# Kernel optimization log

Hardware: AMD Instinct MI355X
Metric: run time of the kernel (lower is better)

Reference implementation:

```python
import jax, jax.numpy as jnp
import numpy as np

BATCH = 2048
K = 64          # num_clusters
D = 128         # latent_dim / cluster_dim
R1 = 1024
OUT_LEN = 512   # output_length
IN_LEN = 512    # input_length
MIN_CLAMP = 0.0


def setup_inputs() -> dict:
    key = jax.random.key(0)
    k1, k2, k3, k4, k5, k6 = jax.random.split(key, 6)
    z = jax.random.normal(k1, (BATCH, 1, D), dtype=jnp.float32)
    u = jax.random.normal(k2, (BATCH, 1, R1), dtype=jnp.float32)
    member = jax.random.uniform(k3, (BATCH, 1, K), dtype=jnp.float32)
    # parameters
    mu = jax.random.uniform(k4, (K, D), dtype=jnp.float32)  # 1 * torch.rand
    sigma_inv = 10.0 * jnp.broadcast_to(jnp.eye(D, dtype=jnp.float32), (K, D, D))  # zeros with diag 10
    # nn.Linear default init: U(-1/sqrt(fan_in), 1/sqrt(fan_in)), weight shape (out, in)
    bound = 1.0 / np.sqrt(R1)
    W_con = jax.random.uniform(k5, (K, OUT_LEN, R1), dtype=jnp.float32, minval=-bound, maxval=bound)
    W_recon = jax.random.uniform(k6, (K, IN_LEN, R1), dtype=jnp.float32, minval=-bound, maxval=bound)
    return {"z": z, "u": u, "member": member, "mu": mu, "sigma_inv": sigma_inv,
            "W_con": W_con, "W_recon": W_recon}


def _compute_psi(z, mu, sigma_inv):
    # z: (B,1,D), mu: (K,D) -> d: (B,K,D)
    d = mu[None, :, :] - z
    # S = sigma_inv @ sigma_inv^T per cluster: (K,D,D)
    S = jnp.einsum('kde,kfe->kdf', sigma_inv, sigma_inv)
    # Mahalanobis: d^T S d per (b,k)
    d2 = jnp.einsum('bkd,kde,bke->bk', d, S, d)
    d2 = jnp.maximum(d2, MIN_CLAMP)
    psi = jax.nn.softmax(-d2, axis=1)  # (B,K)
    return psi


def reference(z, u, member, mu, sigma_inv, W_con, W_recon):
    psi = _compute_psi(z, mu, sigma_inv)          # (B,K)
    u2 = u[:, 0, :]                                # (B,R1)
    # grouped GEMM + abs: per-cluster |Linear(u)|
    y_LLM = jnp.abs(jnp.einsum('bi,koi->bko', u2, W_con))    # (B,K,OUT_LEN)
    x_LLM = jnp.abs(jnp.einsum('bi,koi->bko', u2, W_recon))  # (B,K,IN_LEN)
    mem = member[:, 0, :]                          # (B,K)
    y_con = jnp.einsum('bk,bko->bo', psi, y_LLM)[:, None, :]   # (B,1,OUT_LEN)
    x_recon = jnp.einsum('bk,bko->bo', mem, x_LLM)[:, None, :]  # (B,1,IN_LEN)
    return (y_con, x_recon)
```

## Files before the change

### kernel.cpp

```cpp
#include <hip/hip_runtime.h>
#include <hip/hip_bf16.h>
#include <stdint.h>

typedef __bf16 bf16_t;
typedef __bf16 bf16x8 __attribute__((ext_vector_type(8)));
typedef __bf16 bf16x4 __attribute__((ext_vector_type(4)));
typedef float  v4f    __attribute__((ext_vector_type(4)));
typedef float  f32x4  __attribute__((ext_vector_type(4)));

#define GLDS16(gp, lp)                                                         \
  __builtin_amdgcn_global_load_lds(                                            \
      (__attribute__((address_space(1))) void*)(gp),                           \
      (__attribute__((address_space(3))) void*)(lp), 16, 0, 0)

#define BATCH 2048
#define KEXP  64
#define NOUT  512
#define R1    1024

__global__ __launch_bounds__(256) void cast_u_k(const float* __restrict__ u,
                                                bf16_t* __restrict__ ub) {
  int idx = blockIdx.x * 256 + threadIdx.x;
  float4 v = ((const float4*)u)[idx];
  bf16x4 o;
  o.x = (bf16_t)v.x; o.y = (bf16_t)v.y; o.z = (bf16_t)v.z; o.w = (bf16_t)v.w;
  ((bf16x4*)ub)[idx] = o;
}

__global__ __launch_bounds__(256) void cast_w_k(const float* __restrict__ wcon,
                                                const float* __restrict__ wrec,
                                                bf16_t* __restrict__ wb) {
  const size_t tid = (size_t)blockIdx.x * 256 + threadIdx.x;
#pragma unroll
  for (int it = 0; it < 8; ++it) {
    size_t idx = tid + (size_t)it * (8192u * 256u);
    size_t e = idx << 2;
    int k = (int)(e >> 20);
    int n = (int)((e >> 10) & 1023);
    int i = (int)(e & 1023);
    const float* src = (n < NOUT)
        ? (wcon + (((size_t)k * NOUT + n) << 10) + i)
        : (wrec + (((size_t)k * NOUT + (n - NOUT)) << 10) + i);
    f32x4 v = __builtin_nontemporal_load((const f32x4*)src);
    bf16x4 o;
    o.x = (bf16_t)v.x; o.y = (bf16_t)v.y; o.z = (bf16_t)v.z; o.w = (bf16_t)v.w;
    ((bf16x4*)wb)[idx] = o;
  }
}

__global__ __launch_bounds__(256) void psi_d2_k(const float* __restrict__ z,
                                                const float* __restrict__ mu,
                                                const float* __restrict__ sig,
                                                float* __restrict__ d2g) {
  __shared__ float dv[64][132];
  __shared__ float Ss[16][128];
  const int t = threadIdx.x;
  const int k = blockIdx.x;
  const int b0 = blockIdx.y * 64;

  const float* muk = mu + k * 128;
#pragma unroll
  for (int i = 0; i < 8; ++i) {
    int f4 = i * 256 + t;
    int row = f4 >> 5, c4 = f4 & 31;
    float4 zq = ((const float4*)(z + (size_t)(b0 + row) * 128))[c4];
    float4 mq = ((const float4*)muk)[c4];
    float4 dq;
    dq.x = mq.x - zq.x; dq.y = mq.y - zq.y;
    dq.z = mq.z - zq.z; dq.w = mq.w - zq.w;
    *(float4*)&dv[row][c4 * 4] = dq;
  }

  const int et = t & 15, bt = t >> 4;
  const float* Sk = sig + ((size_t)k << 14);
  float acc[4][8];
#pragma unroll
  for (int j = 0; j < 4; ++j)
#pragma unroll
    for (int i = 0; i < 8; ++i) acc[j][i] = 0.f;

  for (int dblk = 0; dblk < 8; ++dblk) {
    __syncthreads();
#pragma unroll
    for (int i = 0; i < 2; ++i) {
      int f4 = i * 256 + t;
      int row = f4 >> 5, c4 = f4 & 31;
      *(float4*)&Ss[row][c4 * 4] =
          ((const float4*)(Sk + (size_t)(dblk * 16 + row) * 128))[c4];
    }
    __syncthreads();

#pragma unroll
    for (int d4 = 0; d4 < 4; ++d4) {
      float4 a[4];
#pragma unroll
      for (int j = 0; j < 4; ++j)
        a[j] = *(const float4*)&dv[bt * 4 + j][dblk * 16 + d4 * 4];
#pragma unroll
      for (int dd = 0; dd < 4; ++dd) {
        float4 s0 = *(const float4*)&Ss[d4 * 4 + dd][et * 8];
        float4 s1 = *(const float4*)&Ss[d4 * 4 + dd][et * 8 + 4];
        float av[4] = {a[0][dd], a[1][dd], a[2][dd], a[3][dd]};
#pragma unroll
        for (int j = 0; j < 4; ++j) {
          acc[j][0] = fmaf(s0.x, av[j], acc[j][0]);
          acc[j][1] = fmaf(s0.y, av[j], acc[j][1]);
          acc[j][2] = fmaf(s0.z, av[j], acc[j][2]);
          acc[j][3] = fmaf(s0.w, av[j], acc[j][3]);
          acc[j][4] = fmaf(s1.x, av[j], acc[j][4]);
          acc[j][5] = fmaf(s1.y, av[j], acc[j][5]);
          acc[j][6] = fmaf(s1.z, av[j], acc[j][6]);
          acc[j][7] = fmaf(s1.w, av[j], acc[j][7]);
        }
      }
    }
  }

  float v2[4];
#pragma unroll
  for (int j = 0; j < 4; ++j) {
    float s = 0.f;
#pragma unroll
    for (int i = 0; i < 8; ++i) s = fmaf(acc[j][i], acc[j][i], s);
    v2[j] = s;
  }
#pragma unroll
  for (int j = 0; j < 4; ++j) {
    v2[j] += __shfl_xor(v2[j], 1);
    v2[j] += __shfl_xor(v2[j], 2);
    v2[j] += __shfl_xor(v2[j], 4);
    v2[j] += __shfl_xor(v2[j], 8);
  }
  if (et == 0) {
#pragma unroll
    for (int j = 0; j < 4; ++j)
      d2g[(size_t)(b0 + bt * 4 + j) * 64 + k] = v2[j];
  }
}

__global__ __launch_bounds__(256) void psi_sm_k(const float* __restrict__ d2g,
                                                float* __restrict__ psi) {
  const int b = blockIdx.x * 4 + (threadIdx.x >> 6);
  const int lane = threadIdx.x & 63;
  float x = fmaxf(d2g[(size_t)b * 64 + lane], 0.0f);
  float m = x;
  m = fminf(m, __shfl_xor(m, 1));  m = fminf(m, __shfl_xor(m, 2));
  m = fminf(m, __shfl_xor(m, 4));  m = fminf(m, __shfl_xor(m, 8));
  m = fminf(m, __shfl_xor(m, 16)); m = fminf(m, __shfl_xor(m, 32));
  float ex = __expf(m - x);
  float s = ex;
  s += __shfl_xor(s, 1);  s += __shfl_xor(s, 2);  s += __shfl_xor(s, 4);
  s += __shfl_xor(s, 8);  s += __shfl_xor(s, 16); s += __shfl_xor(s, 32);
  psi[(size_t)b * 64 + lane] = ex / s;
}

__global__ __launch_bounds__(256, 2)
void fused_gemm(const bf16_t* __restrict__ ub,
                const bf16_t* __restrict__ wb,
                const float* __restrict__ psi,
                const float* __restrict__ member,
                float* __restrict__ out) {
  __shared__ bf16_t Alds[2][128 * 64];
  __shared__ bf16_t Blds[2][128 * 64];
  __shared__ float  wlds[16][128];

  const int t = threadIdx.x, lane = t & 63, wv = t >> 6;
  const int rr  = blockIdx.x + (blockIdx.y << 4) + (blockIdx.z << 7);
  const int bm0 = ((rr >> 3) & 15) << 7;
  const int n0  = (rr & 7) << 7;
  const int e0  = (rr >> 7) << 4;
  const bool is_y = (n0 < NOUT);
  const float* wsel = is_y ? psi : member;
  const int wm = wv & 1, wn = wv >> 1;
  const int l15 = lane & 15, quad = lane >> 4;
  const int fsw = l15 & 7;

  v4f acc[4][4], oacc[4][4];
#pragma unroll
  for (int mi = 0; mi < 4; ++mi)
#pragma unroll
    for (int ni = 0; ni < 4; ++ni)
#pragma unroll
      for (int r = 0; r < 4; ++r) { acc[mi][ni][r] = 0.f; oacc[mi][ni][r] = 0.f; }

  const int rA = wv * 8 + (lane >> 3);
  const int c8 = (((lane & 7) ^ (lane >> 3)) * 8);
  const bf16_t* au  = ub + (size_t)(bm0 + rA) * R1 + c8;
  const bf16_t* bw0 = wb + (size_t)(n0 + rA) * R1 + c8;

  const int aoff = (wm * 64 + l15) * 64;
  const int boff = (wn * 64 + l15) * 64;
  const int co0 = (quad ^ fsw) * 8;
  const int co1 = ((4 + quad) ^ fsw) * 8;

  auto STAGE = [&](int s2, int p) {
    const int ex2 = e0 + (s2 >> 4);
    const int kk2 = (s2 & 15) << 6;
    const bf16_t* a = au + kk2;
    const bf16_t* b = bw0 + ((size_t)ex2 << 20) + kk2;
    bf16_t* Ad = &Alds[p][wv * 8 * 64];
    bf16_t* Bd = &Blds[p][wv * 8 * 64];
#pragma unroll
    for (int j = 0; j < 4; ++j)
      GLDS16(a + (size_t)(j * 32) * R1, Ad + j * 32 * 64);
#pragma unroll
    for (int j = 0; j < 4; ++j)
      GLDS16(b + (size_t)(j * 32) * R1, Bd + j * 32 * 64);
  };

  {
    const int r = t >> 1, h = (t & 1) * 8;
    const float* src = wsel + (size_t)(bm0 + r) * 64 + e0 + h;
    f32x4 v0 = *(const f32x4*)src;
    f32x4 v1 = *(const f32x4*)(src + 4);
#pragma unroll
    for (int j = 0; j < 4; ++j) { wlds[h + j][r] = v0[j]; wlds[h + 4 + j][r] = v1[j]; }
  }
  STAGE(0, 0);
  STAGE(1, 1);
  asm volatile("s_waitcnt vmcnt(8) lgkmcnt(0)" ::: "memory");
  asm volatile("s_barrier" ::: "memory");

  bf16x8 a0[4], b0[4], a1[4], b1[4];
#pragma unroll
  for (int i = 0; i < 4; ++i) {
    a0[i] = *(const bf16x8*)(&Alds[0][aoff] + i * 16 * 64 + co0);
    b0[i] = *(const bf16x8*)(&Blds[0][boff] + i * 16 * 64 + co0);
  }

  for (int ke = 0; ke < 16; ++ke) {
#pragma unroll 2
    for (int kt = 0; kt < 16; ++kt) {
      const int p = kt & 1;
      const int s = (ke << 4) + kt;
      const bf16_t* Ap = &Alds[p][aoff];
      const bf16_t* Bp = &Blds[p][boff];

#pragma unroll
      for (int i = 0; i < 4; ++i) {
        a1[i] = *(const bf16x8*)(Ap + i * 16 * 64 + co1);
        b1[i] = *(const bf16x8*)(Bp + i * 16 * 64 + co1);
      }
      asm volatile("s_waitcnt lgkmcnt(8)" ::: "memory");
      __builtin_amdgcn_sched_barrier(0);
      __builtin_amdgcn_s_setprio(1);
#pragma unroll
      for (int mi = 0; mi < 4; ++mi)
#pragma unroll
        for (int ni = 0; ni < 4; ++ni)
          acc[mi][ni] = __builtin_amdgcn_mfma_f32_16x16x32_bf16(
              a0[mi], b0[ni], acc[mi][ni], 0, 0, 0);
      __builtin_amdgcn_s_setprio(0);

      asm volatile("s_waitcnt lgkmcnt(0)" ::: "memory");
      asm volatile("s_barrier" ::: "memory");

      int s2 = s + 2; s2 = (s2 > 255) ? 255 : s2;
      STAGE(s2, p);

      asm volatile("s_waitcnt vmcnt(8)" ::: "memory");
      asm volatile("s_barrier" ::: "memory");

      const bf16_t* An = &Alds[p ^ 1][aoff];
      const bf16_t* Bn = &Blds[p ^ 1][boff];
#pragma unroll
      for (int i = 0; i < 4; ++i) {
        a0[i] = *(const bf16x8*)(An + i * 16 * 64 + co0);
        b0[i] = *(const bf16x8*)(Bn + i * 16 * 64 + co0);
      }
      __builtin_amdgcn_s_setprio(1);
#pragma unroll
      for (int mi = 0; mi < 4; ++mi)
#pragma unroll
        for (int ni = 0; ni < 4; ++ni)
          acc[mi][ni] = __builtin_amdgcn_mfma_f32_16x16x32_bf16(
              a1[mi], b1[ni], acc[mi][ni], 0, 0, 0);
      __builtin_amdgcn_s_setprio(0);
    }

#pragma unroll
    for (int mi = 0; mi < 4; ++mi) {
      float wr[4];
#pragma unroll
      for (int r = 0; r < 4; ++r)
        wr[r] = wlds[ke][wm * 64 + mi * 16 + quad * 4 + r];
#pragma unroll
      for (int ni = 0; ni < 4; ++ni)
#pragma unroll
        for (int r = 0; r < 4; ++r) {
          oacc[mi][ni][r] += fabsf(acc[mi][ni][r]) * wr[r];
          acc[mi][ni][r] = 0.f;
        }
    }
  }

  float* obase = is_y ? out : out + (size_t)BATCH * NOUT;
  const int oc = (is_y ? n0 : n0 - NOUT) + wn * 64 + l15;
#pragma unroll
  for (int mi = 0; mi < 4; ++mi)
#pragma unroll
    for (int ni = 0; ni < 4; ++ni)
#pragma unroll
      for (int r = 0; r < 4; ++r) {
        int brow = bm0 + wm * 64 + mi * 16 + quad * 4 + r;
        atomicAdd(&obase[(size_t)brow * NOUT + oc + ni * 16], oacc[mi][ni][r]);
      }
  asm volatile("s_waitcnt vmcnt(0) lgkmcnt(0)" ::: "memory");
}

extern "C" void kernel_launch(void* const* d_in, const int* in_sizes, int n_in,
                              void* d_out, int out_size, void* d_ws, size_t ws_size,
                              hipStream_t stream) {
  const float* z    = (const float*)d_in[0];
  const float* u    = (const float*)d_in[1];
  const float* mem  = (const float*)d_in[2];
  const float* mu   = (const float*)d_in[3];
  const float* sig  = (const float*)d_in[4];
  const float* wcon = (const float*)d_in[5];
  const float* wrec = (const float*)d_in[6];
  float* out = (float*)d_out;

  char* ws = (char*)d_ws;
  bf16_t* ub  = (bf16_t*)ws;
  bf16_t* wb  = (bf16_t*)(ws + ((size_t)4 << 20));
  float*  psw = (float*)(ws + ((size_t)132 << 20));
  float*  d2g = (float*)(ws + ((size_t)132 << 20) + ((size_t)512 << 10));

  hipMemsetAsync(d_out, 0, (size_t)out_size * sizeof(float), stream);
  cast_u_k<<<2048, 256, 0, stream>>>(u, ub);
  cast_w_k<<<8192, 256, 0, stream>>>(wcon, wrec, wb);
  psi_d2_k<<<dim3(64, 32), 256, 0, stream>>>(z, mu, sig, d2g);
  psi_sm_k<<<512, 256, 0, stream>>>(d2g, psw);
  fused_gemm<<<dim3(16, 8, 4), 256, 0, stream>>>(ub, wb, psw, mem, out);
}
```

Before: 642.9 us.

## Load A operand directly from global into registers, dropping A LDS staging

```diff
diff --git a/kernel.cpp b/kernel.cpp
--- a/kernel.cpp
+++ b/kernel.cpp
@@ -160,7 +160,6 @@
                 const float* __restrict__ psi,
                 const float* __restrict__ member,
                 float* __restrict__ out) {
-  __shared__ bf16_t Alds[2][128 * 64];
   __shared__ bf16_t Blds[2][128 * 64];
   __shared__ float  wlds[16][128];
 
@@ -185,27 +184,62 @@
 
   const int rA = wv * 8 + (lane >> 3);
   const int c8 = (((lane & 7) ^ (lane >> 3)) * 8);
-  const bf16_t* au  = ub + (size_t)(bm0 + rA) * R1 + c8;
   const bf16_t* bw0 = wb + (size_t)(n0 + rA) * R1 + c8;
 
-  const int aoff = (wm * 64 + l15) * 64;
+  const bf16_t* uA = ub + (size_t)(bm0 + wm * 64 + l15) * R1 + quad * 8;
+
   const int boff = (wn * 64 + l15) * 64;
   const int co0 = (quad ^ fsw) * 8;
   const int co1 = ((4 + quad) ^ fsw) * 8;
 
-  auto STAGE = [&](int s2, int p) {
+  auto STAGEB = [&](int s2, int p) {
     const int ex2 = e0 + (s2 >> 4);
     const int kk2 = (s2 & 15) << 6;
-    const bf16_t* a = au + kk2;
     const bf16_t* b = bw0 + ((size_t)ex2 << 20) + kk2;
-    bf16_t* Ad = &Alds[p][wv * 8 * 64];
     bf16_t* Bd = &Blds[p][wv * 8 * 64];
-#pragma unroll
-    for (int j = 0; j < 4; ++j)
-      GLDS16(a + (size_t)(j * 32) * R1, Ad + j * 32 * 64);
 #pragma unroll
     for (int j = 0; j < 4; ++j)
       GLDS16(b + (size_t)(j * 32) * R1, Bd + j * 32 * 64);
+  };
+
+  auto LOADA = [&](int s1, bf16x8* af) {
+    const bf16_t* ap = uA + ((s1 & 15) << 6);
+#pragma unroll
+    for (int mi = 0; mi < 4; ++mi) {
+      af[mi]     = *(const bf16x8*)(ap + (size_t)(mi * 16) * R1);
+      af[4 + mi] = *(const bf16x8*)(ap + (size_t)(mi * 16) * R1 + 32);
+    }
+  };
+
+  bf16x8 af0[8], af1[8];
+
+  auto STEP = [&](int s, int p, bf16x8* afc, bf16x8* afn) {
+    const bf16_t* Bp = &Blds[p][boff];
+    bf16x8 bfr[8];
+#pragma unroll
+    for (int i = 0; i < 4; ++i) {
+      bfr[i]     = *(const bf16x8*)(Bp + i * 16 * 64 + co0);
+      bfr[4 + i] = *(const bf16x8*)(Bp + i * 16 * 64 + co1);
+    }
+    int s1 = s + 1; if (s1 > 255) s1 = 255;
+    LOADA(s1, afn);
+    asm volatile("s_waitcnt vmcnt(12) lgkmcnt(0)" ::: "memory");
+    __builtin_amdgcn_sched_barrier(0);
+    asm volatile("s_barrier" ::: "memory");
+    int s2 = s + 2; if (s2 > 255) s2 = 255;
+    STAGEB(s2, p);
+    __builtin_amdgcn_s_setprio(1);
+#pragma unroll
+    for (int ks = 0; ks < 2; ++ks)
+#pragma unroll
+      for (int mi = 0; mi < 4; ++mi)
+#pragma unroll
+        for (int ni = 0; ni < 4; ++ni)
+          acc[mi][ni] = __builtin_amdgcn_mfma_f32_16x16x32_bf16(
+              afc[ks * 4 + mi], bfr[ks * 4 + ni], acc[mi][ni], 0, 0, 0);
+    __builtin_amdgcn_s_setprio(0);
+    asm volatile("s_waitcnt vmcnt(12)" ::: "memory");
+    asm volatile("s_barrier" ::: "memory");
   };
 
   {
@@ -216,68 +250,19 @@
 #pragma unroll
     for (int j = 0; j < 4; ++j) { wlds[h + j][r] = v0[j]; wlds[h + 4 + j][r] = v1[j]; }
   }
-  STAGE(0, 0);
-  STAGE(1, 1);
-  asm volatile("s_waitcnt vmcnt(8) lgkmcnt(0)" ::: "memory");
+  LOADA(0, af0);
+  STAGEB(0, 0);
+  STAGEB(1, 1);
+  asm volatile("s_waitcnt vmcnt(4) lgkmcnt(0)" ::: "memory");
   asm volatile("s_barrier" ::: "memory");
 
-  bf16x8 a0[4], b0[4], a1[4], b1[4];
-#pragma unroll
-  for (int i = 0; i < 4; ++i) {
-    a0[i] = *(const bf16x8*)(&Alds[0][aoff] + i * 16 * 64 + co0);
-    b0[i] = *(const bf16x8*)(&Blds[0][boff] + i * 16 * 64 + co0);
-  }
-
   for (int ke = 0; ke < 16; ++ke) {
+    const int sb = ke << 4;
 #pragma unroll 2
-    for (int kt = 0; kt < 16; ++kt) {
-      const int p = kt & 1;
-      const int s = (ke << 4) + kt;
-      const bf16_t* Ap = &Alds[p][aoff];
-      const bf16_t* Bp = &Blds[p][boff];
-
-#pragma unroll
-      for (int i = 0; i < 4; ++i) {
-        a1[i] = *(const bf16x8*)(Ap + i * 16 * 64 + co1);
-        b1[i] = *(const bf16x8*)(Bp + i * 16 * 64 + co1);
-      }
-      asm volatile("s_waitcnt lgkmcnt(8)" ::: "memory");
-      __builtin_amdgcn_sched_barrier(0);
-      __builtin_amdgcn_s_setprio(1);
-#pragma unroll
-      for (int mi = 0; mi < 4; ++mi)
-#pragma unroll
-        for (int ni = 0; ni < 4; ++ni)
-          acc[mi][ni] = __builtin_amdgcn_mfma_f32_16x16x32_bf16(
-              a0[mi], b0[ni], acc[mi][ni], 0, 0, 0);
-      __builtin_amdgcn_s_setprio(0);
-
-      asm volatile("s_waitcnt lgkmcnt(0)" ::: "memory");
-      asm volatile("s_barrier" ::: "memory");
-
-      int s2 = s + 2; s2 = (s2 > 255) ? 255 : s2;
-      STAGE(s2, p);
-
-      asm volatile("s_waitcnt vmcnt(8)" ::: "memory");
-      asm volatile("s_barrier" ::: "memory");
-
-      const bf16_t* An = &Alds[p ^ 1][aoff];
-      const bf16_t* Bn = &Blds[p ^ 1][boff];
-#pragma unroll
-      for (int i = 0; i < 4; ++i) {
-        a0[i] = *(const bf16x8*)(An + i * 16 * 64 + co0);
-        b0[i] = *(const bf16x8*)(Bn + i * 16 * 64 + co0);
-      }
-      __builtin_amdgcn_s_setprio(1);
-#pragma unroll
-      for (int mi = 0; mi < 4; ++mi)
-#pragma unroll
-        for (int ni = 0; ni < 4; ++ni)
-          acc[mi][ni] = __builtin_amdgcn_mfma_f32_16x16x32_bf16(
-              a1[mi], b1[ni], acc[mi][ni], 0, 0, 0);
-      __builtin_amdgcn_s_setprio(0);
-    }
-
+    for (int kt = 0; kt < 16; kt += 2) {
+      STEP(sb + kt,     0, af0, af1);
+      STEP(sb + kt + 1, 1, af1, af0);
+    }
 #pragma unroll
     for (int mi = 0; mi < 4; ++mi) {
       float wr[4];
```

Measured after the change: 919.1 us. +43.0%, slower.

## Restructure Mahalanobis kernel to read sigma via wave-uniform scalar loads

Applied to the files above, without the earlier changes.

```diff
diff --git a/kernel.cpp b/kernel.cpp
--- a/kernel.cpp
+++ b/kernel.cpp
@@ -52,11 +52,12 @@
                                                 const float* __restrict__ mu,
                                                 const float* __restrict__ sig,
                                                 float* __restrict__ d2g) {
-  __shared__ float dv[64][132];
-  __shared__ float Ss[16][128];
+  __shared__ float dv[64][129];
+  __shared__ float red[4][64];
   const int t = threadIdx.x;
   const int k = blockIdx.x;
   const int b0 = blockIdx.y * 64;
+  const int lane = t & 63;
 
   const float* muk = mu + k * 128;
 #pragma unroll
@@ -65,76 +66,37 @@
     int row = f4 >> 5, c4 = f4 & 31;
     float4 zq = ((const float4*)(z + (size_t)(b0 + row) * 128))[c4];
     float4 mq = ((const float4*)muk)[c4];
-    float4 dq;
-    dq.x = mq.x - zq.x; dq.y = mq.y - zq.y;
-    dq.z = mq.z - zq.z; dq.w = mq.w - zq.w;
-    *(float4*)&dv[row][c4 * 4] = dq;
-  }
-
-  const int et = t & 15, bt = t >> 4;
-  const float* Sk = sig + ((size_t)k << 14);
-  float acc[4][8];
-#pragma unroll
-  for (int j = 0; j < 4; ++j)
-#pragma unroll
-    for (int i = 0; i < 8; ++i) acc[j][i] = 0.f;
-
-  for (int dblk = 0; dblk < 8; ++dblk) {
-    __syncthreads();
-#pragma unroll
-    for (int i = 0; i < 2; ++i) {
-      int f4 = i * 256 + t;
-      int row = f4 >> 5, c4 = f4 & 31;
-      *(float4*)&Ss[row][c4 * 4] =
-          ((const float4*)(Sk + (size_t)(dblk * 16 + row) * 128))[c4];
-    }
-    __syncthreads();
-
-#pragma unroll
-    for (int d4 = 0; d4 < 4; ++d4) {
-      float4 a[4];
-#pragma unroll
-      for (int j = 0; j < 4; ++j)
-        a[j] = *(const float4*)&dv[bt * 4 + j][dblk * 16 + d4 * 4];
-#pragma unroll
-      for (int dd = 0; dd < 4; ++dd) {
-        float4 s0 = *(const float4*)&Ss[d4 * 4 + dd][et * 8];
-        float4 s1 = *(const float4*)&Ss[d4 * 4 + dd][et * 8 + 4];
-        float av[4] = {a[0][dd], a[1][dd], a[2][dd], a[3][dd]};
-#pragma unroll
-        for (int j = 0; j < 4; ++j) {
-          acc[j][0] = fmaf(s0.x, av[j], acc[j][0]);
-          acc[j][1] = fmaf(s0.y, av[j], acc[j][1]);
-          acc[j][2] = fmaf(s0.z, av[j], acc[j][2]);
-          acc[j][3] = fmaf(s0.w, av[j], acc[j][3]);
-          acc[j][4] = fmaf(s1.x, av[j], acc[j][4]);
-          acc[j][5] = fmaf(s1.y, av[j], acc[j][5]);
-          acc[j][6] = fmaf(s1.z, av[j], acc[j][6]);
-          acc[j][7] = fmaf(s1.w, av[j], acc[j][7]);
-        }
-      }
-    }
-  }
-
-  float v2[4];
-#pragma unroll
-  for (int j = 0; j < 4; ++j) {
-    float s = 0.f;
-#pragma unroll
-    for (int i = 0; i < 8; ++i) s = fmaf(acc[j][i], acc[j][i], s);
-    v2[j] = s;
-  }
-#pragma unroll
-  for (int j = 0; j < 4; ++j) {
-    v2[j] += __shfl_xor(v2[j], 1);
-    v2[j] += __shfl_xor(v2[j], 2);
-    v2[j] += __shfl_xor(v2[j], 4);
-    v2[j] += __shfl_xor(v2[j], 8);
-  }
-  if (et == 0) {
-#pragma unroll
-    for (int j = 0; j < 4; ++j)
-      d2g[(size_t)(b0 + bt * 4 + j) * 64 + k] = v2[j];
+    dv[row][c4 * 4 + 0] = mq.x - zq.x;
+    dv[row][c4 * 4 + 1] = mq.y - zq.y;
+    dv[row][c4 * 4 + 2] = mq.z - zq.z;
+    dv[row][c4 * 4 + 3] = mq.w - zq.w;
+  }
+
+  const int e0 = __builtin_amdgcn_readfirstlane((t >> 6) << 5);
+  const float* sk = sig + ((size_t)k << 14) + e0;
+
+  float acc[32];
+#pragma unroll
+  for (int j = 0; j < 32; ++j) acc[j] = 0.f;
+
+  __syncthreads();
+
+#pragma unroll 2
+  for (int d = 0; d < 128; ++d) {
+    float dvd = dv[lane][d];
+    const float* srow = sk + (d << 7);
+#pragma unroll
+    for (int j = 0; j < 32; ++j) acc[j] = fmaf(dvd, srow[j], acc[j]);
+  }
+
+  float s = 0.f;
+#pragma unroll
+  for (int j = 0; j < 32; ++j) s = fmaf(acc[j], acc[j], s);
+  red[t >> 6][lane] = s;
+  __syncthreads();
+  if (t < 64) {
+    float tot = red[0][lane] + red[1][lane] + red[2][lane] + red[3][lane];
+    d2g[(size_t)(b0 + lane) * 64 + k] = tot;
   }
 }
 
```

Result: no change. 634.3 us (-1.3%).
